# Kernel optimization log

Measured on AMD Instinct MI355X. Metric: run time of the kernel, lower is better.

Reference implementation:

```python
import jax, jax.numpy as jnp
import numpy as np

N_NODES = 100000
N_EDGES = 50000
NNZ = 1600000
IN_DIM, HID_DIM, N_CLASSES = 128, 128, 16


def setup_inputs() -> dict:
    key = jax.random.key(0)
    k1, k2, k3, k4, k5 = jax.random.split(key, 5)
    x = jax.random.normal(k1, (N_NODES, IN_DIM), dtype=jnp.float32)
    node_idx = jax.random.randint(k2, (NNZ,), 0, N_NODES, dtype=jnp.int64)
    edge_idx = jax.random.randint(k3, (NNZ,), 0, N_EDGES, dtype=jnp.int64)
    # glorot-ish weights, zero bias (PyG HypergraphConv: Linear(bias=False) + bias Parameter)
    W1 = jax.random.normal(k4, (IN_DIM, HID_DIM), dtype=jnp.float32) * (1.0 / np.sqrt(IN_DIM))
    b1 = jnp.zeros((HID_DIM,), dtype=jnp.float32)
    W2 = jax.random.normal(k5, (HID_DIM, N_CLASSES), dtype=jnp.float32) * (1.0 / np.sqrt(HID_DIM))
    b2 = jnp.zeros((N_CLASSES,), dtype=jnp.float32)
    return {"x": x, "node_idx": node_idx, "edge_idx": edge_idx, "num_edges": N_EDGES,
            "W1": W1, "b1": b1, "W2": W2, "b2": b2}


def hypergraph_conv(x, W, b, node_idx, edge_idx, num_edges):
    """PyG HypergraphConv (no attention, unit hyperedge weights):
       out = D^{-1} H B^{-1} H^T (x W) + b
    implemented as gather -> segment_sum (node->edge) -> gather -> segment_sum (edge->node)."""
    n_nodes = x.shape[0]
    ones = jnp.ones(node_idx.shape[0], dtype=x.dtype)
    deg = jax.ops.segment_sum(ones, node_idx, num_segments=n_nodes)      # D: node degree
    edeg = jax.ops.segment_sum(ones, edge_idx, num_segments=num_edges)   # B: hyperedge size
    Dinv = jnp.where(deg > 0, 1.0 / deg, 0.0)
    Binv = jnp.where(edeg > 0, 1.0 / edeg, 0.0)

    xw = x @ W                                                            # [N, F_out]
    # node -> hyperedge, norm = B^{-1} applied per message (indexed by edge)
    msg_ne = xw[node_idx] * Binv[edge_idx][:, None]                       # [nnz, F_out]
    e_feat = jax.ops.segment_sum(msg_ne, edge_idx, num_segments=num_edges)
    # hyperedge -> node, norm = D^{-1} applied per message (indexed by node)
    msg_en = e_feat[edge_idx] * Dinv[node_idx][:, None]                   # [nnz, F_out]
    out = jax.ops.segment_sum(msg_en, node_idx, num_segments=n_nodes)
    return out + b


def reference(x, node_idx, edge_idx, num_edges, W1, b1, W2, b2):
    # Dropout is inactive in eval mode; model is relu(conv1) -> conv2.
    h = jax.nn.relu(hypergraph_conv(x, W1, b1, node_idx, edge_idx, num_edges))
    return hypergraph_conv(h, W2, b2, node_idx, edge_idx, num_edges)
```

## Files before the change

### kernel.cpp

```cpp
#include <hip/hip_runtime.h>
#include <hip/hip_fp16.h>


#define N_EDGES_C 50000
#define F1 128
#define F2 16
#define CHUNK 4096
#define EBIN_SHIFT 7
#define NBIN_SHIFT 8
#define EBINS 391
#define NBINS 391


__global__ __launch_bounds__(256) void hist_chunk_kernel(
    const int* __restrict__ node_idx, const int* __restrict__ edge_idx,
    int* __restrict__ echunkcnt, int* __restrict__ nchunkcnt, int nnz) {
  __shared__ int ebc[EBINS], nbc[NBINS];
  const int t = threadIdx.x;
  for (int b = t; b < EBINS; b += 256) ebc[b] = 0;
  for (int b = t; b < NBINS; b += 256) nbc[b] = 0;
  __syncthreads();
  const int base = blockIdx.x * CHUNK;
  int end = base + CHUNK; if (end > nnz) end = nnz;
  for (int i = base + t; i < end; i += 256) {
    atomicAdd(&ebc[edge_idx[i] >> EBIN_SHIFT], 1);
    atomicAdd(&nbc[node_idx[i] >> NBIN_SHIFT], 1);
  }
  __syncthreads();
  const int nC = gridDim.x;
  for (int b = t; b < EBINS; b += 256) echunkcnt[b * nC + blockIdx.x] = ebc[b];
  for (int b = t; b < NBINS; b += 256) nchunkcnt[b * nC + blockIdx.x] = nbc[b];
}

__global__ __launch_bounds__(256) void cscan_p1_kernel(
    const int* __restrict__ ecc, const int* __restrict__ ncc,
    int* __restrict__ epart, int* __restrict__ npart,
    int Le, int Ln, int nbE) {
  __shared__ int red[256];
  const int t = threadIdx.x;
  const int b = blockIdx.x;
  const int* src; int L; int* dst; int bb;
  if (b < nbE) { src = ecc; L = Le; dst = epart; bb = b; }
  else         { src = ncc; L = Ln; dst = npart; bb = b - nbE; }
  int base = bb * 1024 + t * 4;
  int s = 0;
#pragma unroll
  for (int j = 0; j < 4; ++j) { int i = base + j; if (i < L) s += src[i]; }
  red[t] = s;
  __syncthreads();
  for (int d = 128; d > 0; d >>= 1) {
    if (t < d) red[t] += red[t + d];
    __syncthreads();
  }
  if (t == 0) dst[bb] = red[0];
}

__global__ __launch_bounds__(256) void cscan_p2_kernel(
    int* __restrict__ epart, int* __restrict__ npart,
    int* __restrict__ ebinbase, int* __restrict__ nbinbase,
    int nbE, int nbN, int nnz) {
  __shared__ int se[256], sn[256];
  const int t = threadIdx.x;
  se[t] = (t < nbE) ? epart[t] : 0;
  sn[t] = (t < nbN) ? npart[t] : 0;
  __syncthreads();
  for (int d = 1; d < 256; d <<= 1) {
    int ve = (t >= d) ? se[t - d] : 0;
    int vn = (t >= d) ? sn[t - d] : 0;
    __syncthreads();
    se[t] += ve; sn[t] += vn;
    __syncthreads();
  }
  if (t < nbE) epart[t] = (t > 0) ? se[t - 1] : 0;
  if (t < nbN) npart[t] = (t > 0) ? sn[t - 1] : 0;
  if (t == 0) { ebinbase[EBINS] = nnz; nbinbase[NBINS] = nnz; }
}

__global__ __launch_bounds__(256) void cscan_p3_kernel(
    const int* __restrict__ ecc, const int* __restrict__ ncc,
    const int* __restrict__ epart, const int* __restrict__ npart,
    int* __restrict__ erunoff, int* __restrict__ nrunoff,
    int* __restrict__ ebinbase, int* __restrict__ nbinbase,
    int Le, int Ln, int nbE, int nC) {
  __shared__ int red[256];
  const int t = threadIdx.x;
  const int b = blockIdx.x;
  const int* src; const int* part; int L; int* ro; int* bba; int bb;
  if (b < nbE) { src = ecc; part = epart; L = Le; ro = erunoff; bba = ebinbase; bb = b; }
  else         { src = ncc; part = npart; L = Ln; ro = nrunoff; bba = nbinbase; bb = b - nbE; }
  int base = bb * 1024 + t * 4;
  int v[4]; int s = 0;
#pragma unroll
  for (int j = 0; j < 4; ++j) { int i = base + j; v[j] = (i < L) ? src[i] : 0; s += v[j]; }
  red[t] = s;
  __syncthreads();
  for (int d = 1; d < 256; d <<= 1) {
    int x = (t >= d) ? red[t - d] : 0;
    __syncthreads();
    red[t] += x;
    __syncthreads();
  }
  int run = part[bb] + ((t > 0) ? red[t - 1] : 0);
#pragma unroll
  for (int j = 0; j < 4; ++j) {
    int i = base + j;
    if (i < L) {
      ro[i] = run;
      if (i % nC == 0) bba[i / nC] = run;
      run += v[j];
    }
  }
}

__global__ __launch_bounds__(256) void stage_kernel(
    const int* __restrict__ node_idx, const int* __restrict__ edge_idx,
    const int* __restrict__ erunoff, const int* __restrict__ nrunoff,
    int2* __restrict__ epairs, int2* __restrict__ npairs, int nnz) {
  __shared__ int ecur[EBINS], ncur[NBINS];
  const int t = threadIdx.x;
  const int nC = gridDim.x;
  for (int b = t; b < EBINS; b += 256) ecur[b] = erunoff[b * nC + blockIdx.x];
  for (int b = t; b < NBINS; b += 256) ncur[b] = nrunoff[b * nC + blockIdx.x];
  __syncthreads();
  const int base = blockIdx.x * CHUNK;
  int end = base + CHUNK; if (end > nnz) end = nnz;
  for (int i = base + t; i < end; i += 256) {
    int e = edge_idx[i];
    int n = node_idx[i];
    int p = atomicAdd(&ecur[e >> EBIN_SHIFT], 1);
    epairs[p] = make_int2(e, n);
    int q = atomicAdd(&ncur[n >> NBIN_SHIFT], 1);
    npairs[q] = make_int2(n, e);
  }
}

__global__ __launch_bounds__(256) void bin_scatter_kernel(
    const int2* __restrict__ epairs, const int2* __restrict__ npairs,
    const int* __restrict__ ebinbase, const int* __restrict__ nbinbase,
    int* __restrict__ eoff, int* __restrict__ noff,
    int* __restrict__ enbr, int* __restrict__ nnbr,
    int n_edges, int n_nodes) {
  __shared__ int cnt[256];
  __shared__ int scn[256];
  const int bid = blockIdx.x;
  const int t = threadIdx.x;
  if (bid < EBINS) {
    const int e0 = bid << EBIN_SHIFT;
    const int ne = min(1 << EBIN_SHIFT, n_edges - e0);
    const int beg = ebinbase[bid], end = ebinbase[bid + 1];
    if (t < 128) cnt[t] = 0;
    __syncthreads();
    for (int j = beg + t; j < end; j += 256) atomicAdd(&cnt[epairs[j].x & 127], 1);
    __syncthreads();
    if (t < 128) scn[t] = cnt[t];
    __syncthreads();
    for (int d = 1; d < 128; d <<= 1) {
      int x = 0;
      if (t < 128 && t >= d) x = scn[t - d];
      __syncthreads();
      if (t < 128) scn[t] += x;
      __syncthreads();
    }
    int pos0 = 0;
    if (t < 128) {
      int excl = (t > 0) ? scn[t - 1] : 0;
      pos0 = beg + excl;
      if (t < ne) eoff[e0 + t] = pos0;
    }
    __syncthreads();
    if (t < 128) scn[t] = pos0;
    __syncthreads();
    for (int j = beg + t; j < end; j += 256) {
      int2 p = epairs[j];
      int pos = atomicAdd(&scn[p.x & 127], 1);
      enbr[pos] = p.y;
    }
    if (bid == EBINS - 1 && t == 0) eoff[n_edges] = end;
  } else {
    const int b = bid - EBINS;
    const int n0 = b << NBIN_SHIFT;
    const int nn = min(1 << NBIN_SHIFT, n_nodes - n0);
    const int beg = nbinbase[b], end = nbinbase[b + 1];
    cnt[t] = 0;
    __syncthreads();
    for (int j = beg + t; j < end; j += 256) atomicAdd(&cnt[npairs[j].x & 255], 1);
    __syncthreads();
    scn[t] = cnt[t];
    __syncthreads();
    for (int d = 1; d < 256; d <<= 1) {
      int x = (t >= d) ? scn[t - d] : 0;
      __syncthreads();
      scn[t] += x;
      __syncthreads();
    }
    int excl = (t > 0) ? scn[t - 1] : 0;
    int pos0 = beg + excl;
    if (t < nn) noff[n0 + t] = pos0;
    __syncthreads();
    scn[t] = pos0;
    __syncthreads();
    for (int j = beg + t; j < end; j += 256) {
      int2 p = npairs[j];
      int pos = atomicAdd(&scn[p.x & 255], 1);
      nnbr[pos] = p.y;
    }
    if (bid == EBINS + NBINS - 1 && t == 0) noff[n_nodes] = end;
  }
}


__global__ __launch_bounds__(256) void gemm1_kernel(
    const float* __restrict__ A, const float* __restrict__ B,
    __half* __restrict__ C16, int M) {
  __shared__ float xs[128][36];
  __shared__ float wsh[32][128];

  const int t = threadIdx.x;
  const int tx = t & 15;
  const int ty = t >> 4;
  const int bm = blockIdx.x * 128;

  float acc[8][8];
#pragma unroll
  for (int i = 0; i < 8; ++i)
#pragma unroll
    for (int j = 0; j < 8; ++j) acc[i][j] = 0.f;

  for (int kt = 0; kt < 4; ++kt) {
#pragma unroll
    for (int i = 0; i < 4; ++i) {
      int lin = i * 256 + t;
      int row = lin >> 3;
      int c4 = lin & 7;
      int grow = bm + row;
      float4 v = make_float4(0.f, 0.f, 0.f, 0.f);
      if (grow < M) v = *(const float4*)(A + (size_t)grow * 128 + kt * 32 + c4 * 4);
      *(float4*)&xs[row][c4 * 4] = v;
    }
#pragma unroll
    for (int i = 0; i < 4; ++i) {
      int lin = i * 256 + t;
      int k = lin >> 5;
      int c4 = lin & 31;
      *(float4*)&wsh[k][c4 * 4] = *(const float4*)(B + (size_t)(kt * 32 + k) * 128 + c4 * 4);
    }
    __syncthreads();

#pragma unroll 4
    for (int k = 0; k < 32; ++k) {
      float a[8], b[8];
#pragma unroll
      for (int j = 0; j < 4; ++j) {
        a[j]     = xs[ty * 4 + j][k];
        a[4 + j] = xs[ty * 4 + 64 + j][k];
      }
      float4 b0 = *(const float4*)&wsh[k][tx * 4];
      float4 b1 = *(const float4*)&wsh[k][tx * 4 + 64];
      b[0] = b0.x; b[1] = b0.y; b[2] = b0.z; b[3] = b0.w;
      b[4] = b1.x; b[5] = b1.y; b[6] = b1.z; b[7] = b1.w;
#pragma unroll
      for (int i = 0; i < 8; ++i)
#pragma unroll
        for (int j = 0; j < 8; ++j) acc[i][j] = fmaf(a[i], b[j], acc[i][j]);
    }
    __syncthreads();
  }

#pragma unroll
  for (int i = 0; i < 8; ++i) {
    int row = (i < 4) ? (ty * 4 + i) : (ty * 4 + 64 + (i - 4));
    int grow = bm + row;
    if (grow < M) {
      __half2* rp = (__half2*)(C16 + (size_t)grow * 128);
      rp[tx * 2]          = __floats2half2_rn(acc[i][0], acc[i][1]);
      rp[tx * 2 + 1]      = __floats2half2_rn(acc[i][2], acc[i][3]);
      rp[32 + tx * 2]     = __floats2half2_rn(acc[i][4], acc[i][5]);
      rp[32 + tx * 2 + 1] = __floats2half2_rn(acc[i][6], acc[i][7]);
    }
  }
}


__device__ __forceinline__ void acc_h8(float* ax, float4 v) {
  const __half2* h = (const __half2*)&v;
#pragma unroll
  for (int q = 0; q < 4; ++q) {
    float2 f = __half22float2(h[q]);
    ax[2 * q] += f.x; ax[2 * q + 1] += f.y;
  }
}

__global__ __launch_bounds__(256) void edge_agg128_kernel(
    const float4* __restrict__ feat,
    const int* __restrict__ nbr, const int* __restrict__ off,
    float4* __restrict__ outf, int nseg) {
  int w = (blockIdx.x * 256 + threadIdx.x) >> 6;
  if (w >= nseg) return;
  const int lane = threadIdx.x & 63;
  const int r = lane >> 4;
  const int f = lane & 15;
  int beg = off[w], end = off[w + 1];
  float ax[8];
#pragma unroll
  for (int i = 0; i < 8; ++i) ax[i] = 0.f;
  int k = beg + r;
  for (; k + 12 < end; k += 16) {
    int n0 = nbr[k], n1 = nbr[k + 4], n2 = nbr[k + 8], n3 = nbr[k + 12];
    float4 v0 = feat[(size_t)n0 * 16 + f];
    float4 v1 = feat[(size_t)n1 * 16 + f];
    float4 v2 = feat[(size_t)n2 * 16 + f];
    float4 v3 = feat[(size_t)n3 * 16 + f];
    acc_h8(ax, v0); acc_h8(ax, v1); acc_h8(ax, v2); acc_h8(ax, v3);
  }
  for (; k < end; k += 4) acc_h8(ax, feat[(size_t)nbr[k] * 16 + f]);
#pragma unroll
  for (int i = 0; i < 8; ++i) {
    ax[i] += __shfl_xor(ax[i], 16, 64);
    ax[i] += __shfl_xor(ax[i], 32, 64);
  }
  if (r == 0) {
    float inv = (end > beg) ? 1.f / (float)(end - beg) : 0.f;
    union { float4 f4; __half2 h[4]; } u;
#pragma unroll
    for (int q = 0; q < 4; ++q)
      u.h[q] = __floats2half2_rn(ax[2 * q] * inv, ax[2 * q + 1] * inv);
    outf[(size_t)w * 16 + f] = u.f4;
  }
}

__global__ __launch_bounds__(256) void node_agg128_kernel(
    const float4* __restrict__ feat,
    const int* __restrict__ nbr, const int* __restrict__ off,
    const float* __restrict__ bias,
    float4* __restrict__ outf, int nseg) {
  int w = (blockIdx.x * 256 + threadIdx.x) >> 6;
  if (w >= nseg) return;
  const int lane = threadIdx.x & 63;
  const int r = lane >> 4;
  const int f = lane & 15;
  int beg = off[w], end = off[w + 1];
  float ax[8];
#pragma unroll
  for (int i = 0; i < 8; ++i) ax[i] = 0.f;
  int k = beg + r;
  for (; k + 12 < end; k += 16) {
    int e0 = nbr[k], e1 = nbr[k + 4], e2 = nbr[k + 8], e3 = nbr[k + 12];
    float4 v0 = feat[(size_t)e0 * 16 + f];
    float4 v1 = feat[(size_t)e1 * 16 + f];
    float4 v2 = feat[(size_t)e2 * 16 + f];
    float4 v3 = feat[(size_t)e3 * 16 + f];
    acc_h8(ax, v0); acc_h8(ax, v1); acc_h8(ax, v2); acc_h8(ax, v3);
  }
  for (; k < end; k += 4) acc_h8(ax, feat[(size_t)nbr[k] * 16 + f]);
#pragma unroll
  for (int i = 0; i < 8; ++i) {
    ax[i] += __shfl_xor(ax[i], 16, 64);
    ax[i] += __shfl_xor(ax[i], 32, 64);
  }
  if (r == 0) {
    float inv = (end > beg) ? 1.f / (float)(end - beg) : 0.f;
    float4 blo = ((const float4*)bias)[2 * f];
    float4 bhi = ((const float4*)bias)[2 * f + 1];
    float bb[8] = {blo.x, blo.y, blo.z, blo.w, bhi.x, bhi.y, bhi.z, bhi.w};
    union { float4 f4; __half2 h[4]; } u;
#pragma unroll
    for (int q = 0; q < 4; ++q) {
      float hx = fmaxf(ax[2 * q] * inv + bb[2 * q], 0.f);
      float hy = fmaxf(ax[2 * q + 1] * inv + bb[2 * q + 1], 0.f);
      u.h[q] = __floats2half2_rn(hx, hy);
    }
    outf[(size_t)w * 16 + f] = u.f4;
  }
}


__global__ __launch_bounds__(256) void gemm2_kernel(
    const __half* __restrict__ H16, const float* __restrict__ W2,
    __half2* __restrict__ O16, int M) {
  __shared__ float ws2[128 * 16];
  const int t = threadIdx.x;
#pragma unroll
  for (int i = 0; i < 8; ++i) ws2[i * 256 + t] = W2[i * 256 + t];
  __syncthreads();

  int r0 = blockIdx.x * 512 + t;
  int r1 = r0 + 256;
  bool v0 = r0 < M, v1 = r1 < M;
  const __half2* h0 = (const __half2*)(H16 + (size_t)r0 * 128);
  const __half2* h1 = (const __half2*)(H16 + (size_t)r1 * 128);

  float4 acc0[4], acc1[4];
#pragma unroll
  for (int q = 0; q < 4; ++q) {
    acc0[q] = make_float4(0.f, 0.f, 0.f, 0.f);
    acc1[q] = make_float4(0.f, 0.f, 0.f, 0.f);
  }

  for (int k4 = 0; k4 < 32; ++k4) {
    float2 f00 = make_float2(0.f, 0.f), f01 = make_float2(0.f, 0.f);
    float2 f10 = make_float2(0.f, 0.f), f11 = make_float2(0.f, 0.f);
    if (v0) { f00 = __half22float2(h0[2 * k4]); f01 = __half22float2(h0[2 * k4 + 1]); }
    if (v1) { f10 = __half22float2(h1[2 * k4]); f11 = __half22float2(h1[2 * k4 + 1]); }
    const float a0s[4] = {f00.x, f00.y, f01.x, f01.y};
    const float a1s[4] = {f10.x, f10.y, f11.x, f11.y};
#pragma unroll
    for (int j = 0; j < 4; ++j) {
      int k = k4 * 4 + j;
#pragma unroll
      for (int q = 0; q < 4; ++q) {
        float4 b = *(const float4*)&ws2[k * 16 + q * 4];
        acc0[q].x = fmaf(a0s[j], b.x, acc0[q].x);
        acc0[q].y = fmaf(a0s[j], b.y, acc0[q].y);
        acc0[q].z = fmaf(a0s[j], b.z, acc0[q].z);
        acc0[q].w = fmaf(a0s[j], b.w, acc0[q].w);
        acc1[q].x = fmaf(a1s[j], b.x, acc1[q].x);
        acc1[q].y = fmaf(a1s[j], b.y, acc1[q].y);
        acc1[q].z = fmaf(a1s[j], b.z, acc1[q].z);
        acc1[q].w = fmaf(a1s[j], b.w, acc1[q].w);
      }
    }
  }
  if (v0) {
    __half2* op = O16 + (size_t)r0 * 8;
#pragma unroll
    for (int q = 0; q < 4; ++q) {
      op[q * 2]     = __floats2half2_rn(acc0[q].x, acc0[q].y);
      op[q * 2 + 1] = __floats2half2_rn(acc0[q].z, acc0[q].w);
    }
  }
  if (v1) {
    __half2* op = O16 + (size_t)r1 * 8;
#pragma unroll
    for (int q = 0; q < 4; ++q) {
      op[q * 2]     = __floats2half2_rn(acc1[q].x, acc1[q].y);
      op[q * 2 + 1] = __floats2half2_rn(acc1[q].z, acc1[q].w);
    }
  }
}


__global__ __launch_bounds__(256) void edge_agg16_kernel(
    const __half* __restrict__ feat, const int* __restrict__ nbr,
    const int* __restrict__ off, float* __restrict__ outf, int nseg) {
  int gid = blockIdx.x * 256 + threadIdx.x;
  int seg = gid >> 4;
  int c = gid & 15;
  if (seg >= nseg) return;
  int beg = off[seg], end = off[seg + 1];
  float a0 = 0.f, a1 = 0.f, a2 = 0.f, a3 = 0.f;
  int j = beg;
  for (; j + 8 <= end; j += 8) {
    int n0 = nbr[j],     n1 = nbr[j + 1], n2 = nbr[j + 2], n3 = nbr[j + 3];
    int n4 = nbr[j + 4], n5 = nbr[j + 5], n6 = nbr[j + 6], n7 = nbr[j + 7];
    float v0 = __half2float(feat[(size_t)n0 * 16 + c]);
    float v1 = __half2float(feat[(size_t)n1 * 16 + c]);
    float v2 = __half2float(feat[(size_t)n2 * 16 + c]);
    float v3 = __half2float(feat[(size_t)n3 * 16 + c]);
    float v4 = __half2float(feat[(size_t)n4 * 16 + c]);
    float v5 = __half2float(feat[(size_t)n5 * 16 + c]);
    float v6 = __half2float(feat[(size_t)n6 * 16 + c]);
    float v7 = __half2float(feat[(size_t)n7 * 16 + c]);
    a0 += v0 + v4; a1 += v1 + v5; a2 += v2 + v6; a3 += v3 + v7;
  }
  for (; j < end; ++j) a0 += __half2float(feat[(size_t)nbr[j] * 16 + c]);
  float inv = (end > beg) ? 1.f / (float)(end - beg) : 0.f;
  outf[(size_t)seg * 16 + c] = ((a0 + a1) + (a2 + a3)) * inv;
}

__global__ __launch_bounds__(256) void node_agg16_kernel(
    const float* __restrict__ feat, const int* __restrict__ nbr,
    const int* __restrict__ off, const float* __restrict__ bias,
    float* __restrict__ outf, int nseg) {
  int gid = blockIdx.x * 256 + threadIdx.x;
  int seg = gid >> 4;
  int c = gid & 15;
  if (seg >= nseg) return;
  int beg = off[seg], end = off[seg + 1];
  float a0 = 0.f, a1 = 0.f, a2 = 0.f, a3 = 0.f;
  int j = beg;
  for (; j + 8 <= end; j += 8) {
    int n0 = nbr[j],     n1 = nbr[j + 1], n2 = nbr[j + 2], n3 = nbr[j + 3];
    int n4 = nbr[j + 4], n5 = nbr[j + 5], n6 = nbr[j + 6], n7 = nbr[j + 7];
    float v0 = feat[(size_t)n0 * 16 + c];
    float v1 = feat[(size_t)n1 * 16 + c];
    float v2 = feat[(size_t)n2 * 16 + c];
    float v3 = feat[(size_t)n3 * 16 + c];
    float v4 = feat[(size_t)n4 * 16 + c];
    float v5 = feat[(size_t)n5 * 16 + c];
    float v6 = feat[(size_t)n6 * 16 + c];
    float v7 = feat[(size_t)n7 * 16 + c];
    a0 += v0 + v4; a1 += v1 + v5; a2 += v2 + v6; a3 += v3 + v7;
  }
  for (; j < end; ++j) a0 += feat[(size_t)nbr[j] * 16 + c];
  float inv = (end > beg) ? 1.f / (float)(end - beg) : 0.f;
  outf[(size_t)seg * 16 + c] = ((a0 + a1) + (a2 + a3)) * inv + bias[c];
}


extern "C" void kernel_launch(void* const* d_in, const int* in_sizes, int n_in,
                              void* d_out, int out_size, void* d_ws, size_t ws_size,
                              hipStream_t stream) {
  const float* x        = (const float*)d_in[0];
  const int*   node_idx = (const int*)d_in[1];
  const int*   edge_idx = (const int*)d_in[2];
  const float* W1 = (const float*)d_in[4];
  const float* b1 = (const float*)d_in[5];
  const float* W2 = (const float*)d_in[6];
  const float* b2 = (const float*)d_in[7];
  float* out = (float*)d_out;

  const int n_nodes = in_sizes[0] / F1;
  const int nnz     = in_sizes[1];
  const int n_edges = N_EDGES_C;
  const int nC      = (nnz + CHUNK - 1) / CHUNK;
  const int Le      = EBINS * nC;
  const int Ln      = NBINS * nC;
  const int nbE     = (Le + 1023) / 1024;
  const int nbN     = (Ln + 1023) / 1024;

  char* ws = (char*)d_ws;
  int2*    epairs = (int2*)(ws + 0);
  int2*    npairs = (int2*)(ws + 12800000);
  __half*  h16    = (__half*)(ws + 0);
  __half*  xw16   = (__half*)(ws + 25600000);
  __half*  ef16   = (__half*)(ws + 51200000);
  __half*  hw216  = (__half*)(ws + 64000000);
  float*   ef2    = (float*)(ws + 70400000);
  int*     enbr   = (int*)(ws + 73600000);
  int*     nnbr   = (int*)(ws + 80000000);
  int*     eoff   = (int*)(ws + 86400000);
  int*     noff   = (int*)(ws + 86600008);
  int*     echunkcnt = (int*)(ws + 87000016);
  int*     nchunkcnt = (int*)(ws + 87611540);
  int*     erunoff   = (int*)(ws + 88223064);
  int*     nrunoff   = (int*)(ws + 88834588);
  int*     ebinbase  = (int*)(ws + 89446112);
  int*     nbinbase  = (int*)(ws + 89447680);
  int*     epart     = (int*)(ws + 89449248);
  int*     npart     = (int*)(ws + 89450272);

  hist_chunk_kernel<<<nC, 256, 0, stream>>>(node_idx, edge_idx,
                                            echunkcnt, nchunkcnt, nnz);
  cscan_p1_kernel<<<nbE + nbN, 256, 0, stream>>>(echunkcnt, nchunkcnt,
                                                 epart, npart, Le, Ln, nbE);
  cscan_p2_kernel<<<1, 256, 0, stream>>>(epart, npart, ebinbase, nbinbase,
                                         nbE, nbN, nnz);
  cscan_p3_kernel<<<nbE + nbN, 256, 0, stream>>>(echunkcnt, nchunkcnt,
                                                 epart, npart, erunoff, nrunoff,
                                                 ebinbase, nbinbase, Le, Ln, nbE, nC);
  stage_kernel<<<nC, 256, 0, stream>>>(node_idx, edge_idx, erunoff, nrunoff,
                                       epairs, npairs, nnz);
  bin_scatter_kernel<<<EBINS + NBINS, 256, 0, stream>>>(epairs, npairs,
                                                        ebinbase, nbinbase,
                                                        eoff, noff, enbr, nnbr,
                                                        n_edges, n_nodes);

  gemm1_kernel<<<(n_nodes + 127) / 128, 256, 0, stream>>>(x, W1, xw16, n_nodes);
  edge_agg128_kernel<<<(n_edges * 64 + 255) / 256, 256, 0, stream>>>(
      (const float4*)xw16, enbr, eoff, (float4*)ef16, n_edges);
  node_agg128_kernel<<<(n_nodes * 64 + 255) / 256, 256, 0, stream>>>(
      (const float4*)ef16, nnbr, noff, b1, (float4*)h16, n_nodes);

  gemm2_kernel<<<(n_nodes + 511) / 512, 256, 0, stream>>>(h16, W2,
                                                          (__half2*)hw216, n_nodes);
  edge_agg16_kernel<<<(n_edges * 16 + 255) / 256, 256, 0, stream>>>(
      hw216, enbr, eoff, ef2, n_edges);
  node_agg16_kernel<<<(n_nodes * 16 + 255) / 256, 256, 0, stream>>>(
      ef2, nnbr, noff, b2, out, n_nodes);
}
```

Measured before the change: 405.0 us.

## Use fp16 MFMA matrix cores for first-layer GEMM with transposed half weights

Replaces the fp32 FMA register-tiled GEMM for x@W1 with a matrix-core version using mfma_f32_16x16x32_f16. A small kernel transposes W1 and converts it to fp16; x is converted to fp16 when loaded into LDS. The output is staged through LDS so global stores are coalesced. This cuts the ALU cost of the GEMM, but x and W1 are now rounded to fp16 before multiplication, and one extra small kernel launch is added.

```diff
diff --git a/kernel.cpp b/kernel.cpp
--- a/kernel.cpp
+++ b/kernel.cpp
@@ -10,6 +10,9 @@
 #define NBIN_SHIFT 8
 #define EBINS 391
 #define NBINS 391
+
+typedef __attribute__((ext_vector_type(8))) _Float16 half8;
+typedef __attribute__((ext_vector_type(4))) float f32x4;
 
 
 __global__ __launch_bounds__(256) void hist_chunk_kernel(
@@ -209,74 +212,83 @@
 }
 
 
+__global__ __launch_bounds__(256) void w1t_kernel(
+    const float* __restrict__ W1, __half* __restrict__ W1t) {
+  int i = blockIdx.x * 256 + threadIdx.x;
+  int n = i >> 7, k = i & 127;
+  W1t[i] = __float2half(W1[k * 128 + n]);
+}
+
+
 __global__ __launch_bounds__(256) void gemm1_kernel(
-    const float* __restrict__ A, const float* __restrict__ B,
+    const float* __restrict__ A, const __half* __restrict__ W1t16,
     __half* __restrict__ C16, int M) {
-  __shared__ float xs[128][36];
-  __shared__ float wsh[32][128];
-
-  const int t = threadIdx.x;
-  const int tx = t & 15;
-  const int ty = t >> 4;
-  const int bm = blockIdx.x * 128;
-
-  float acc[8][8];
-#pragma unroll
-  for (int i = 0; i < 8; ++i)
-#pragma unroll
-    for (int j = 0; j < 8; ++j) acc[i][j] = 0.f;
-
+  __shared__ _Float16 As[64 * 136];
+  __shared__ _Float16 Bs[128 * 136];
+  const int t = threadIdx.x;
+  const int bm = blockIdx.x * 64;
+
+#pragma unroll
+  for (int i = 0; i < 8; ++i) {
+    int lin = i * 256 + t;
+    int row = lin >> 5;
+    int c4 = lin & 31;
+    int grow = bm + row;
+    float4 v = make_float4(0.f, 0.f, 0.f, 0.f);
+    if (grow < M) v = *(const float4*)(A + (size_t)grow * 128 + c4 * 4);
+    _Float16* dst = &As[row * 136 + c4 * 4];
+    dst[0] = (_Float16)v.x; dst[1] = (_Float16)v.y;
+    dst[2] = (_Float16)v.z; dst[3] = (_Float16)v.w;
+  }
+#pragma unroll
+  for (int i = 0; i < 8; ++i) {
+    int lin = i * 256 + t;
+    int n = lin >> 4;
+    int c = lin & 15;
+    *(float4*)&Bs[n * 136 + c * 8] = *(const float4*)(W1t16 + n * 128 + c * 8);
+  }
+  __syncthreads();
+
+  const int w = t >> 6;
+  const int lane = t & 63;
+  const int l16 = lane & 15;
+  const int quad = lane >> 4;
+
+  f32x4 acc[8];
+#pragma unroll
+  for (int n = 0; n < 8; ++n) acc[n] = (f32x4){0.f, 0.f, 0.f, 0.f};
+
+  const _Float16* arow = &As[(w * 16 + l16) * 136 + quad * 8];
+#pragma unroll
   for (int kt = 0; kt < 4; ++kt) {
-#pragma unroll
-    for (int i = 0; i < 4; ++i) {
-      int lin = i * 256 + t;
-      int row = lin >> 3;
-      int c4 = lin & 7;
-      int grow = bm + row;
-      float4 v = make_float4(0.f, 0.f, 0.f, 0.f);
-      if (grow < M) v = *(const float4*)(A + (size_t)grow * 128 + kt * 32 + c4 * 4);
-      *(float4*)&xs[row][c4 * 4] = v;
-    }
-#pragma unroll
-    for (int i = 0; i < 4; ++i) {
-      int lin = i * 256 + t;
-      int k = lin >> 5;
-      int c4 = lin & 31;
-      *(float4*)&wsh[k][c4 * 4] = *(const float4*)(B + (size_t)(kt * 32 + k) * 128 + c4 * 4);
-    }
-    __syncthreads();
-
-#pragma unroll 4
-    for (int k = 0; k < 32; ++k) {
-      float a[8], b[8];
-#pragma unroll
-      for (int j = 0; j < 4; ++j) {
-        a[j]     = xs[ty * 4 + j][k];
-        a[4 + j] = xs[ty * 4 + 64 + j][k];
-      }
-      float4 b0 = *(const float4*)&wsh[k][tx * 4];
-      float4 b1 = *(const float4*)&wsh[k][tx * 4 + 64];
-      b[0] = b0.x; b[1] = b0.y; b[2] = b0.z; b[3] = b0.w;
-      b[4] = b1.x; b[5] = b1.y; b[6] = b1.z; b[7] = b1.w;
-#pragma unroll
-      for (int i = 0; i < 8; ++i)
-#pragma unroll
-        for (int j = 0; j < 8; ++j) acc[i][j] = fmaf(a[i], b[j], acc[i][j]);
-    }
-    __syncthreads();
-  }
-
-#pragma unroll
-  for (int i = 0; i < 8; ++i) {
-    int row = (i < 4) ? (ty * 4 + i) : (ty * 4 + 64 + (i - 4));
+    half8 a = *(const half8*)(arow + kt * 32);
+#pragma unroll
+    for (int n = 0; n < 8; ++n) {
+      half8 b = *(const half8*)&Bs[(n * 16 + l16) * 136 + kt * 32 + quad * 8];
+      acc[n] = __builtin_amdgcn_mfma_f32_16x16x32_f16(a, b, acc[n], 0, 0, 0);
+    }
+  }
+  __syncthreads();
+
+#pragma unroll
+  for (int n = 0; n < 8; ++n) {
+#pragma unroll
+    for (int r = 0; r < 4; ++r) {
+      int row = w * 16 + quad * 4 + r;
+      int col = n * 16 + l16;
+      As[row * 136 + col] = (_Float16)acc[n][r];
+    }
+  }
+  __syncthreads();
+
+#pragma unroll
+  for (int i = 0; i < 4; ++i) {
+    int lin = i * 256 + t;
+    int row = lin >> 4;
+    int c = lin & 15;
     int grow = bm + row;
-    if (grow < M) {
-      __half2* rp = (__half2*)(C16 + (size_t)grow * 128);
-      rp[tx * 2]          = __floats2half2_rn(acc[i][0], acc[i][1]);
-      rp[tx * 2 + 1]      = __floats2half2_rn(acc[i][2], acc[i][3]);
-      rp[32 + tx * 2]     = __floats2half2_rn(acc[i][4], acc[i][5]);
-      rp[32 + tx * 2 + 1] = __floats2half2_rn(acc[i][6], acc[i][7]);
-    }
+    if (grow < M)
+      *(float4*)(C16 + (size_t)grow * 128 + c * 8) = *(const float4*)&As[row * 136 + c * 8];
   }
 }
 
@@ -538,6 +550,9 @@
   int*     nbinbase  = (int*)(ws + 89447680);
   int*     epart     = (int*)(ws + 89449248);
   int*     npart     = (int*)(ws + 89450272);
+  __half*  w1t16     = (__half*)(ws + 89451520);
+
+  w1t_kernel<<<64, 256, 0, stream>>>(W1, w1t16);
 
   hist_chunk_kernel<<<nC, 256, 0, stream>>>(node_idx, edge_idx,
                                             echunkcnt, nchunkcnt, nnz);
@@ -555,7 +570,7 @@
                                                         eoff, noff, enbr, nnbr,
                                                         n_edges, n_nodes);
 
-  gemm1_kernel<<<(n_nodes + 127) / 128, 256, 0, stream>>>(x, W1, xw16, n_nodes);
+  gemm1_kernel<<<(n_nodes + 63) / 64, 256, 0, stream>>>(x, w1t16, xw16, n_nodes);
   edge_agg128_kernel<<<(n_edges * 64 + 255) / 256, 256, 0, stream>>>(
       (const float4*)xw16, enbr, eoff, (float4*)ef16, n_edges);
   node_agg128_kernel<<<(n_nodes * 64 + 255) / 256, 256, 0, stream>>>(
```

New measurement: 370.4 us. -8.5%, faster.
